# Kernel tuning notes

Measured on AMD Instinct MI355X. Metric: run time of the kernel, lower is better.

The kernel has to match this reference:

```python
import jax, jax.numpy as jnp
import numpy as np

B, K, N = 8, 4, 131072
T = B * K * N  # upper bound on packed length
NEG_IDLE = -1e8   # logit value forced when slot is idle
NEG_FILL = -1000.0  # padded-output fill value for logits


def setup_inputs() -> dict:
    key = jax.random.key(0)
    k1, k2, k3, k4, k5, k6 = jax.random.split(key, 6)
    return {
        "rgb": jax.random.normal(k1, (T, 3), dtype=jnp.float32),
        "logits_surface": jax.random.normal(k2, (T, 1), dtype=jnp.float32),
        "logits_air": jax.random.normal(k3, (T, 1), dtype=jnp.float32),
        "mask_surface": jax.random.bernoulli(k4, 0.5, (B, K, N)),
        "mask_air": jax.random.bernoulli(k5, 0.5, (B, K, N)),
        "idle_states": jax.random.uniform(k6, (B, K), dtype=jnp.float32),
    }


def reference(rgb, logits_surface, logits_air, mask_surface, mask_air, idle_states):
    # Packed arrays are laid out in flattened (b, k, n) order: the packed index of a
    # masked element equals the count of True entries preceding it -> cumsum - 1.
    Bb, Kk, Nn = mask_surface.shape
    scale = (1.0 - idle_states)[:, :, None, None]          # [B,K,1,1]
    idle = idle_states[:, :, None, None]                   # [B,K,1,1]

    ms_flat = mask_surface.reshape(-1)
    idx_s = (jnp.cumsum(ms_flat.astype(jnp.int32)) - 1).reshape(Bb, Kk, Nn)
    ms = mask_surface[..., None]                           # [B,K,N,1]

    rgb_g = jnp.take(rgb, idx_s, axis=0)                   # [B,K,N,3]
    rgb_out = jnp.where(ms, rgb_g * scale, 0.0)

    ls_g = jnp.take(logits_surface, idx_s, axis=0)         # [B,K,N,1]
    logits_surface_out = jnp.where(ms, ls_g * scale + idle * NEG_IDLE, NEG_FILL)

    ma_flat = mask_air.reshape(-1)
    idx_a = (jnp.cumsum(ma_flat.astype(jnp.int32)) - 1).reshape(Bb, Kk, Nn)
    ma = mask_air[..., None]
    la_g = jnp.take(logits_air, idx_a, axis=0)             # [B,K,N,1]
    logits_air_out = jnp.where(ma, la_g * scale + idle * NEG_IDLE, NEG_FILL)

    return rgb_out, logits_surface_out, logits_air_out
```

## Files before the change

kernel.cpp:

```cpp
#include <hip/hip_runtime.h>
#include <stdint.h>

#define T_TOTAL  4194304
#define NEG_IDLE (-100000000.0f)
#define NEG_FILL (-1000.0f)

#define BLOCK  256
#define EPT    8
#define EPB    (BLOCK * EPT)
#define NCHUNK (T_TOTAL / EPB)

#define WS_PACKED_OFF  (NCHUNK * sizeof(unsigned long long))
#define WS_PREFIX_OFF  (WS_PACKED_OFF + (size_t)NCHUNK * BLOCK * sizeof(unsigned short))

typedef unsigned u32x4 __attribute__((ext_vector_type(4)));

__device__ __forceinline__ unsigned decode8_i32(const u32x4* p) {
    const u32x4 a = __builtin_nontemporal_load(p);
    const u32x4 b = __builtin_nontemporal_load(p + 1);
    return (a.x ? 1u : 0u) | (a.y ? 2u : 0u) | (a.z ? 4u : 0u) | (a.w ? 8u : 0u)
         | (b.x ? 16u : 0u) | (b.y ? 32u : 0u) | (b.z ? 64u : 0u) | (b.w ? 128u : 0u);
}

__global__ __launch_bounds__(BLOCK) void reduce_pack_kernel(
    const u32x4* __restrict__ ms,
    const u32x4* __restrict__ ma,
    unsigned long long* __restrict__ sums,
    unsigned short* __restrict__ packed)
{
    const int blk  = blockIdx.x;
    const int tid  = threadIdx.x;
    const int lane = tid & 63;
    const int wave = tid >> 6;
    const size_t e = (size_t)blk * EPB + (size_t)tid * EPT;

    const unsigned bits_s = decode8_i32(ms + (e >> 2));
    const unsigned bits_a = decode8_i32(ma + (e >> 2));
    packed[blk * BLOCK + tid] = (unsigned short)(bits_s | (bits_a << 8));

    unsigned long long v =
        ((unsigned long long)(unsigned)__popc(bits_a) << 32) | (unsigned)__popc(bits_s);
    #pragma unroll
    for (int d = 32; d; d >>= 1) v += __shfl_down(v, d, 64);

    __shared__ unsigned long long w[BLOCK / 64];
    if (lane == 0) w[wave] = v;
    __syncthreads();
    if (tid == 0) sums[blk] = w[0] + w[1] + w[2] + w[3];
}

__global__ __launch_bounds__(1024) void scan_kernel(
    const unsigned long long* __restrict__ sums,
    unsigned long long* __restrict__ prefix)
{
    const int tid  = threadIdx.x;
    const int lane = tid & 63;
    const int wave = tid >> 6;

    const unsigned long long a = sums[2 * tid];
    const unsigned long long b = sums[2 * tid + 1];
    const unsigned long long s = a + b;

    unsigned long long incl = s;
    #pragma unroll
    for (int d = 1; d < 64; d <<= 1) {
        unsigned long long t = __shfl_up(incl, d, 64);
        if (lane >= d) incl += t;
    }

    __shared__ unsigned long long wtot[16];
    if (lane == 63) wtot[wave] = incl;
    __syncthreads();
    unsigned long long prior = 0;
    #pragma unroll
    for (int w = 0; w < 16; ++w)
        if (w < wave) prior += wtot[w];

    const unsigned long long excl = prior + (incl - s);
    prefix[2 * tid]     = excl;
    prefix[2 * tid + 1] = excl + a;
}

__global__ __launch_bounds__(BLOCK) void scatter_kernel(
    const float* __restrict__ rgb,
    const float* __restrict__ ls,
    const float* __restrict__ la,
    const unsigned long long* __restrict__ prefix,
    const unsigned short* __restrict__ packed,
    const float* __restrict__ idle_states,
    float* __restrict__ out)
{
    __shared__ float stage[3 * EPB];
    __shared__ int   wtot[BLOCK / 64];

    const int bid  = blockIdx.x;
    const int role = bid >> 11;
    const int blk  = bid & (NCHUNK - 1);
    const int tid  = threadIdx.x;
    const int lane = tid & 63;
    const int wave = tid >> 6;
    const size_t base = (size_t)blk * EPB + (size_t)tid * EPT;

    const unsigned pw   = packed[blk * BLOCK + tid];
    const unsigned bits = (role == 2) ? (pw >> 8) : (pw & 0xffu);
    const int c = __popc(bits);

    const unsigned long long pre64 = prefix[blk];
    const int S0 = (role == 2) ? (int)(pre64 >> 32) : (int)(pre64 & 0xffffffffull);

    int incl = c;
    #pragma unroll
    for (int d = 1; d < 64; d <<= 1) {
        const int t = __shfl_up(incl, d, 64);
        if (lane >= d) incl += t;
    }
    int excl = incl - c;

    if (lane == 63) wtot[wave] = incl;
    __syncthreads();
    #pragma unroll
    for (int w = 0; w < BLOCK / 64; ++w)
        if (w < wave) excl += wtot[w];
    const int tot = wtot[0] + wtot[1] + wtot[2] + wtot[3];

    if (role == 0) {
        const float* src = rgb + (size_t)3 * S0;
        const int n = 3 * tot;
        for (int i = tid; i < n; i += BLOCK) stage[i] = src[i];
    } else {
        const float* src = ((role == 1) ? ls : la) + S0;
        for (int i = tid; i < tot; i += BLOCK) stage[i] = src[i];
    }
    __syncthreads();

    int loc[EPT];
    #pragma unroll
    for (int j = 0; j < EPT; ++j)
        loc[j] = excl + __popc(bits & ((1u << j) - 1u));

    const float idle      = idle_states[blk >> 6];
    const float scale     = 1.0f - idle;
    const float idle_term = idle * NEG_IDLE;

    if (role == 0) {
        float r[3 * EPT];
        #pragma unroll
        for (int j = 0; j < EPT; ++j) {
            r[3 * j + 0] = stage[3 * loc[j] + 0];
            r[3 * j + 1] = stage[3 * loc[j] + 1];
            r[3 * j + 2] = stage[3 * loc[j] + 2];
        }
        #pragma unroll
        for (int j = 0; j < EPT; ++j) {
            const bool bs = (bits >> j) & 1u;
            r[3 * j + 0] = bs ? r[3 * j + 0] * scale : 0.0f;
            r[3 * j + 1] = bs ? r[3 * j + 1] * scale : 0.0f;
            r[3 * j + 2] = bs ? r[3 * j + 2] * scale : 0.0f;
        }
        float4* dst = (float4*)(out + base * 3);
        #pragma unroll
        for (int j = 0; j < 6; ++j) dst[j] = ((const float4*)r)[j];
    } else {
        float v[EPT];
        #pragma unroll
        for (int j = 0; j < EPT; ++j) v[j] = stage[loc[j]];
        #pragma unroll
        for (int j = 0; j < EPT; ++j) {
            const bool b = (bits >> j) & 1u;
            v[j] = b ? (v[j] * scale + idle_term) : NEG_FILL;
        }
        float4* dst = (float4*)(out + (size_t)(2 + role) * T_TOTAL + base);
        dst[0] = ((const float4*)v)[0];
        dst[1] = ((const float4*)v)[1];
    }
}

extern "C" void kernel_launch(void* const* d_in, const int* in_sizes, int n_in,
                              void* d_out, int out_size, void* d_ws, size_t ws_size,
                              hipStream_t stream) {
    const float* rgb  = (const float*)d_in[0];
    const float* ls   = (const float*)d_in[1];
    const float* la   = (const float*)d_in[2];
    const u32x4* ms   = (const u32x4*)d_in[3];
    const u32x4* ma   = (const u32x4*)d_in[4];
    const float* idle = (const float*)d_in[5];
    float* out = (float*)d_out;

    unsigned long long* sums   = (unsigned long long*)d_ws;
    unsigned short*     packed = (unsigned short*)((uint8_t*)d_ws + WS_PACKED_OFF);
    unsigned long long* prefix = (unsigned long long*)((uint8_t*)d_ws + WS_PREFIX_OFF);

    reduce_pack_kernel<<<NCHUNK, BLOCK, 0, stream>>>(ms, ma, sums, packed);
    scan_kernel<<<1, 1024, 0, stream>>>(sums, prefix);
    scatter_kernel<<<3 * NCHUNK, BLOCK, 0, stream>>>(rgb, ls, la, prefix, packed,
                                                     idle, out);
}
```

Baseline: 194.7 us.

## Fuse scatter roles into one block and gather directly without LDS staging

The three per-output scatter roles (rgb, surface logits, air logits) are merged into a single block that runs one 64-bit packed scan covering both masks. The shared-memory staging of the packed source range is removed. Each thread now reads its eight candidate logits as two unaligned float4 loads and selects values with a popcount-based pick, while rgb is gathered straight from global memory. This removes two extra scans, the LDS round trip and a third of the launched blocks. In exchange it adds unaligned and less coalesced global loads, and reads up to eight elements past a thread's valid range near the packed end.

```diff
diff --git a/kernel.cpp b/kernel.cpp
--- a/kernel.cpp
+++ b/kernel.cpp
@@ -14,12 +14,19 @@
 #define WS_PREFIX_OFF  (WS_PACKED_OFF + (size_t)NCHUNK * BLOCK * sizeof(unsigned short))
 
 typedef unsigned u32x4 __attribute__((ext_vector_type(4)));
+typedef float f4u __attribute__((ext_vector_type(4), aligned(4)));
 
 __device__ __forceinline__ unsigned decode8_i32(const u32x4* p) {
     const u32x4 a = __builtin_nontemporal_load(p);
     const u32x4 b = __builtin_nontemporal_load(p + 1);
     return (a.x ? 1u : 0u) | (a.y ? 2u : 0u) | (a.z ? 4u : 0u) | (a.w ? 8u : 0u)
          | (b.x ? 16u : 0u) | (b.y ? 32u : 0u) | (b.z ? 64u : 0u) | (b.w ? 128u : 0u);
+}
+
+__device__ __forceinline__ float pick8(const f4u a, const f4u b, int pc) {
+    const float lo = (pc & 1) ? ((pc & 2) ? a.w : a.y) : ((pc & 2) ? a.z : a.x);
+    const float hi = (pc & 1) ? ((pc & 2) ? b.w : b.y) : ((pc & 2) ? b.z : b.x);
+    return (pc & 4) ? hi : lo;
 }
 
 __global__ __launch_bounds__(BLOCK) void reduce_pack_kernel(
@@ -90,89 +97,88 @@
     const float* __restrict__ idle_states,
     float* __restrict__ out)
 {
-    __shared__ float stage[3 * EPB];
-    __shared__ int   wtot[BLOCK / 64];
-
-    const int bid  = blockIdx.x;
-    const int role = bid >> 11;
-    const int blk  = bid & (NCHUNK - 1);
+    const int blk  = blockIdx.x;
     const int tid  = threadIdx.x;
     const int lane = tid & 63;
     const int wave = tid >> 6;
     const size_t base = (size_t)blk * EPB + (size_t)tid * EPT;
 
-    const unsigned pw   = packed[blk * BLOCK + tid];
-    const unsigned bits = (role == 2) ? (pw >> 8) : (pw & 0xffu);
-    const int c = __popc(bits);
-
-    const unsigned long long pre64 = prefix[blk];
-    const int S0 = (role == 2) ? (int)(pre64 >> 32) : (int)(pre64 & 0xffffffffull);
-
-    int incl = c;
+    const unsigned p = packed[blk * BLOCK + tid];
+    const unsigned bits_s = p & 0xffu;
+    const unsigned bits_a = p >> 8;
+
+    const unsigned long long pre = prefix[blk];
+
+    const unsigned long long pk =
+        ((unsigned long long)(unsigned)__popc(bits_a) << 32) | (unsigned)__popc(bits_s);
+    unsigned long long incl = pk;
     #pragma unroll
     for (int d = 1; d < 64; d <<= 1) {
-        const int t = __shfl_up(incl, d, 64);
+        unsigned long long t = __shfl_up(incl, d, 64);
         if (lane >= d) incl += t;
     }
-    int excl = incl - c;
-
+    unsigned long long excl = incl - pk;
+
+    __shared__ unsigned long long wtot[BLOCK / 64];
     if (lane == 63) wtot[wave] = incl;
     __syncthreads();
     #pragma unroll
     for (int w = 0; w < BLOCK / 64; ++w)
         if (w < wave) excl += wtot[w];
-    const int tot = wtot[0] + wtot[1] + wtot[2] + wtot[3];
-
-    if (role == 0) {
-        const float* src = rgb + (size_t)3 * S0;
-        const int n = 3 * tot;
-        for (int i = tid; i < n; i += BLOCK) stage[i] = src[i];
-    } else {
-        const float* src = ((role == 1) ? ls : la) + S0;
-        for (int i = tid; i < tot; i += BLOCK) stage[i] = src[i];
-    }
-    __syncthreads();
-
-    int loc[EPT];
+
+    const int idx_s0 = (int)((pre + excl) & 0xffffffffULL);
+    const int idx_a0 = (int)((pre + excl) >> 32);
+
+    int is_[EPT];
     #pragma unroll
     for (int j = 0; j < EPT; ++j)
-        loc[j] = excl + __popc(bits & ((1u << j) - 1u));
+        is_[j] = idx_s0 + __popc(bits_s & ((1u << j) - 1u));
+
+    float r[3 * EPT];
+    #pragma unroll
+    for (int j = 0; j < EPT; ++j) {
+        const float* rp = rgb + (size_t)is_[j] * 3;
+        r[3 * j + 0] = rp[0];
+        r[3 * j + 1] = rp[1];
+        r[3 * j + 2] = rp[2];
+    }
+
+    const f4u* pls_src = (const f4u*)(ls + idx_s0);
+    const f4u* pla_src = (const f4u*)(la + idx_a0);
+    const f4u ls_a = pls_src[0], ls_b = pls_src[1];
+    const f4u la_a = pla_src[0], la_b = pla_src[1];
 
     const float idle      = idle_states[blk >> 6];
     const float scale     = 1.0f - idle;
     const float idle_term = idle * NEG_IDLE;
 
-    if (role == 0) {
-        float r[3 * EPT];
-        #pragma unroll
-        for (int j = 0; j < EPT; ++j) {
-            r[3 * j + 0] = stage[3 * loc[j] + 0];
-            r[3 * j + 1] = stage[3 * loc[j] + 1];
-            r[3 * j + 2] = stage[3 * loc[j] + 2];
-        }
-        #pragma unroll
-        for (int j = 0; j < EPT; ++j) {
-            const bool bs = (bits >> j) & 1u;
-            r[3 * j + 0] = bs ? r[3 * j + 0] * scale : 0.0f;
-            r[3 * j + 1] = bs ? r[3 * j + 1] * scale : 0.0f;
-            r[3 * j + 2] = bs ? r[3 * j + 2] * scale : 0.0f;
-        }
-        float4* dst = (float4*)(out + base * 3);
-        #pragma unroll
-        for (int j = 0; j < 6; ++j) dst[j] = ((const float4*)r)[j];
-    } else {
-        float v[EPT];
-        #pragma unroll
-        for (int j = 0; j < EPT; ++j) v[j] = stage[loc[j]];
-        #pragma unroll
-        for (int j = 0; j < EPT; ++j) {
-            const bool b = (bits >> j) & 1u;
-            v[j] = b ? (v[j] * scale + idle_term) : NEG_FILL;
-        }
-        float4* dst = (float4*)(out + (size_t)(2 + role) * T_TOTAL + base);
-        dst[0] = ((const float4*)v)[0];
-        dst[1] = ((const float4*)v)[1];
-    }
+    float sv[EPT], av[EPT];
+    #pragma unroll
+    for (int j = 0; j < EPT; ++j) {
+        const bool bs = (bits_s >> j) & 1u;
+        const bool ba = (bits_a >> j) & 1u;
+        const int pcs = __popc(bits_s & ((1u << j) - 1u));
+        const int pca = __popc(bits_a & ((1u << j) - 1u));
+        const float lsv = pick8(ls_a, ls_b, pcs);
+        const float lav = pick8(la_a, la_b, pca);
+        r[3 * j + 0] = bs ? r[3 * j + 0] * scale : 0.0f;
+        r[3 * j + 1] = bs ? r[3 * j + 1] * scale : 0.0f;
+        r[3 * j + 2] = bs ? r[3 * j + 2] * scale : 0.0f;
+        sv[j] = bs ? (lsv * scale + idle_term) : NEG_FILL;
+        av[j] = ba ? (lav * scale + idle_term) : NEG_FILL;
+    }
+
+    float4* prgb = (float4*)(out + base * 3);
+    #pragma unroll
+    for (int j = 0; j < 6; ++j) prgb[j] = ((const float4*)r)[j];
+
+    float4* pls = (float4*)(out + (size_t)3 * T_TOTAL + base);
+    pls[0] = ((const float4*)sv)[0];
+    pls[1] = ((const float4*)sv)[1];
+
+    float4* pla = (float4*)(out + (size_t)4 * T_TOTAL + base);
+    pla[0] = ((const float4*)av)[0];
+    pla[1] = ((const float4*)av)[1];
 }
 
 extern "C" void kernel_launch(void* const* d_in, const int* in_sizes, int n_in,
@@ -192,6 +198,6 @@
 
     reduce_pack_kernel<<<NCHUNK, BLOCK, 0, stream>>>(ms, ma, sums, packed);
     scan_kernel<<<1, 1024, 0, stream>>>(sums, prefix);
-    scatter_kernel<<<3 * NCHUNK, BLOCK, 0, stream>>>(rgb, ls, la, prefix, packed,
-                                                     idle, out);
-}
+    scatter_kernel<<<NCHUNK, BLOCK, 0, stream>>>(rgb, ls, la, prefix, packed,
+                                                 idle, out);
+}
```

New measurement: 188.3 us. 1.03x faster.
